# Optimization experiments

Hardware: AMD Instinct MI355X
Metric: run time of the kernel (lower is better)

The kernel has to match this reference:

```python
import jax, jax.numpy as jnp
import numpy as np

OUT, IN = 4096, 4096
B, S = 4, 2048


def setup_inputs() -> dict:
    key = jax.random.key(0)
    k1, k2, k3, k4 = jax.random.split(key, 4)
    x = jax.random.normal(k1, (B, S, IN), dtype=jnp.float32)
    # signed int8 values, stored as int32 for portability
    weight_int8 = jax.random.randint(k2, (OUT, IN), -128, 128, dtype=jnp.int32)
    # per-row dequant scale (positive, small)
    scale = jax.random.uniform(k3, (OUT,), dtype=jnp.float32) * 0.01 + 1e-4
    bias = jax.random.normal(k4, (OUT,), dtype=jnp.float32)
    return {"x": x, "weight_int8": weight_int8, "scale": scale, "bias": bias}


def reference(x, weight_int8, scale, bias):
    # dequantize: int8 -> fp, per-row scale (scale.view(-1,1) branch)
    w = weight_int8.astype(x.dtype) * scale[:, None]          # [OUT, IN]
    # F.linear(x, w, bias) = x @ w.T + bias
    out = jnp.einsum("bsi,oi->bso", x, w) + bias               # [B, S, OUT]
    return out
```

## Files before the change

kernel.cpp:

```cpp
#include <hip/hip_runtime.h>
#include <hip/hip_bf16.h>
#include <stdint.h>


#define M_TOT 8192
#define N_TOT 4096
#define K_TOT 4096

#define BM 128
#define BN 128
#define BK 32

typedef uint32_t u32;
typedef __attribute__((ext_vector_type(4))) float f32x4;
typedef __attribute__((ext_vector_type(8))) __bf16 bf16x8;

#define GLOBAL_AS __attribute__((address_space(1)))
#define LDS_AS __attribute__((address_space(3)))
#define ASYNC_COPY16(gp, lp) \
  __builtin_amdgcn_global_load_lds((GLOBAL_AS void*)(gp), (LDS_AS void*)(lp), 16, 0, 0)

__device__ __forceinline__ uint16_t bf16_rne(float f) {
  u32 u = __builtin_bit_cast(u32, f);
  u32 r = u + 0x7FFFu + ((u >> 16) & 1u);
  return (uint16_t)(r >> 16);
}

__global__ __launch_bounds__(256) void cvt_x_kernel(const float* __restrict__ x,
                                                    uint16_t* __restrict__ hi,
                                                    uint16_t* __restrict__ lo,
                                                    int n4) {
  int idx = blockIdx.x * blockDim.x + threadIdx.x;
  int stride = gridDim.x * blockDim.x;
  for (int i = idx; i < n4; i += stride) {
    float4 v = reinterpret_cast<const float4*>(x)[i];
    float fv[4] = {v.x, v.y, v.z, v.w};
    uint16_t hh[4], ll[4];
#pragma unroll
    for (int j = 0; j < 4; ++j) {
      uint16_t hb = bf16_rne(fv[j]);
      float hf = __builtin_bit_cast(float, (u32)hb << 16);
      hh[j] = hb;
      ll[j] = bf16_rne(fv[j] - hf);
    }
    uint2 hv, lv;
    hv.x = (u32)hh[0] | ((u32)hh[1] << 16);
    hv.y = (u32)hh[2] | ((u32)hh[3] << 16);
    lv.x = (u32)ll[0] | ((u32)ll[1] << 16);
    lv.y = (u32)ll[2] | ((u32)ll[3] << 16);
    reinterpret_cast<uint2*>(hi)[i] = hv;
    reinterpret_cast<uint2*>(lo)[i] = lv;
  }
}

__global__ __launch_bounds__(256) void cvt_w_kernel(const int* __restrict__ w,
                                                    uint16_t* __restrict__ wb,
                                                    int n4) {
  int idx = blockIdx.x * blockDim.x + threadIdx.x;
  int stride = gridDim.x * blockDim.x;
  for (int i = idx; i < n4; i += stride) {
    int4 v = reinterpret_cast<const int4*>(w)[i];
    uint16_t r0 = (uint16_t)(__builtin_bit_cast(u32, (float)v.x) >> 16);
    uint16_t r1 = (uint16_t)(__builtin_bit_cast(u32, (float)v.y) >> 16);
    uint16_t r2 = (uint16_t)(__builtin_bit_cast(u32, (float)v.z) >> 16);
    uint16_t r3 = (uint16_t)(__builtin_bit_cast(u32, (float)v.w) >> 16);
    uint2 rv;
    rv.x = (u32)r0 | ((u32)r1 << 16);
    rv.y = (u32)r2 | ((u32)r3 << 16);
    reinterpret_cast<uint2*>(wb)[i] = rv;
  }
}

__global__ __launch_bounds__(256, 2) void gemm_kernel(
    const uint16_t* __restrict__ xhi, const uint16_t* __restrict__ xlo,
    const uint16_t* __restrict__ wb, const float* __restrict__ scale,
    const float* __restrict__ bias, float* __restrict__ out) {
  __shared__ __align__(16) uint16_t sAhi[BM * BK];
  __shared__ __align__(16) uint16_t sAlo[BM * BK];
  __shared__ __align__(16) uint16_t sW[BN * BK];

  const int NBX = N_TOT / BN;
  const int NWG = (M_TOT / BM) * NBX;
  int wg = (int)blockIdx.x;
  wg = (wg & 7) * (NWG >> 3) + (wg >> 3);
  const int by = wg / NBX;
  const int bx = wg % NBX;
  const int m0 = by * BM;
  const int n0 = bx * BN;

  const int tid = (int)threadIdx.x;
  const int lane = tid & 63;
  const int wid = tid >> 6;
  const int wm = (wid >> 1) * 64;
  const int wn = (wid & 1) * 64;

  const int srow = lane >> 2;
  const int scol = (lane & 3) * 8;

  const int fr = lane & 15;
  const int fk = (lane >> 4) * 8;

  f32x4 acc[4][4] = {};

  for (int ks = 0; ks < K_TOT / BK; ++ks) {
    const int k0 = ks * BK;
    __syncthreads();
#pragma unroll
    for (int i = 0; i < 2; ++i) {
      const int chunk = wid * 2 + i;
      const int row = chunk * 16 + srow;
      const size_t ga = (size_t)(m0 + row) * K_TOT + (size_t)(k0 + scol);
      const size_t gw = (size_t)(n0 + row) * K_TOT + (size_t)(k0 + scol);
      ASYNC_COPY16(xhi + ga, &sAhi[chunk * 16 * BK]);
      ASYNC_COPY16(xlo + ga, &sAlo[chunk * 16 * BK]);
      ASYNC_COPY16(wb + gw, &sW[chunk * 16 * BK]);
    }
    __syncthreads();

    bf16x8 ah[4], al[4], bf[4];
#pragma unroll
    for (int m = 0; m < 4; ++m) {
      const int r = wm + m * 16 + fr;
      ah[m] = *reinterpret_cast<const bf16x8*>(&sAhi[r * BK + fk]);
      al[m] = *reinterpret_cast<const bf16x8*>(&sAlo[r * BK + fk]);
    }
#pragma unroll
    for (int n = 0; n < 4; ++n) {
      const int c = wn + n * 16 + fr;
      bf[n] = *reinterpret_cast<const bf16x8*>(&sW[c * BK + fk]);
    }
#pragma unroll
    for (int m = 0; m < 4; ++m) {
#pragma unroll
      for (int n = 0; n < 4; ++n) {
        acc[m][n] = __builtin_amdgcn_mfma_f32_16x16x32_bf16(ah[m], bf[n], acc[m][n], 0, 0, 0);
        acc[m][n] = __builtin_amdgcn_mfma_f32_16x16x32_bf16(al[m], bf[n], acc[m][n], 0, 0, 0);
      }
    }
  }

  const int fq = lane >> 4;
#pragma unroll
  for (int n = 0; n < 4; ++n) {
    const int col = n0 + wn + n * 16 + (lane & 15);
    const float sc = scale[col];
    const float bi = bias[col];
#pragma unroll
    for (int m = 0; m < 4; ++m) {
      const int rbase = m0 + wm + m * 16 + fq * 4;
#pragma unroll
      for (int j = 0; j < 4; ++j) {
        out[(size_t)(rbase + j) * N_TOT + col] = acc[m][n][j] * sc + bi;
      }
    }
  }
}

extern "C" void kernel_launch(void* const* d_in, const int* in_sizes, int n_in,
                              void* d_out, int out_size, void* d_ws, size_t ws_size,
                              hipStream_t stream) {
  const float* x = (const float*)d_in[0];
  const int* w8 = (const int*)d_in[1];
  const float* scale = (const float*)d_in[2];
  const float* bias = (const float*)d_in[3];
  float* out = (float*)d_out;

  uint16_t* xhi = (uint16_t*)d_ws;
  uint16_t* xlo = xhi + (size_t)M_TOT * K_TOT;
  uint16_t* wbf = xlo + (size_t)M_TOT * K_TOT;

  const int x_n4 = (M_TOT * K_TOT) / 4;
  const int w_n4 = (N_TOT * K_TOT) / 4;

  cvt_x_kernel<<<2048, 256, 0, stream>>>(x, xhi, xlo, x_n4);
  cvt_w_kernel<<<1024, 256, 0, stream>>>(w8, wbf, w_n4);

  const int nwg = (M_TOT / BM) * (N_TOT / BN);
  gemm_kernel<<<nwg, 256, 0, stream>>>(xhi, xlo, wbf, scale, bias, out);
}
```

Baseline: 827.3 us.

## Rewrite GEMM as 8-wave 256x256 double-buffered pipeline with swizzled LDS

The GEMM kernel moves from 128x128x32 tiles with 4 waves to 256x256x64 tiles with 8 waves in a 128KB LDS double buffer. The hi and lo halves of x become one concatenated K dimension of 8192, so each MFMA pass reads a single A operand. Global-to-LDS async loads for the next tiles are interleaved with four MFMA quadrants, using explicit waitcnt, barriers and setprio, and the LDS layout is XOR-swizzled to avoid bank conflicts. The goal is more reuse per loaded tile and overlap of memory traffic with matrix math. The cost is a fragile, hand-scheduled pipeline, the weight tiles being loaded twice, and only one workgroup fitting per CU.

```diff
diff --git a/kernel.cpp b/kernel.cpp
--- a/kernel.cpp
+++ b/kernel.cpp
@@ -6,10 +6,11 @@
 #define M_TOT 8192
 #define N_TOT 4096
 #define K_TOT 4096
-
-#define BM 128
-#define BN 128
-#define BK 32
+#define KE    8192
+#define BM 256
+#define BN 256
+#define BK 64
+#define NT (KE / BK)
 
 typedef uint32_t u32;
 typedef __attribute__((ext_vector_type(4))) float f32x4;
@@ -17,8 +18,17 @@
 
 #define GLOBAL_AS __attribute__((address_space(1)))
 #define LDS_AS __attribute__((address_space(3)))
-#define ASYNC_COPY16(gp, lp) \
-  __builtin_amdgcn_global_load_lds((GLOBAL_AS void*)(gp), (LDS_AS void*)(lp), 16, 0, 0)
+#define ASYNC16(gp, lp) \
+  __builtin_amdgcn_global_load_lds((const GLOBAL_AS void*)(gp), (LDS_AS void*)(lp), 16, 0, 0)
+
+#define FENCE asm volatile("" ::: "memory")
+#define BARRIER __builtin_amdgcn_s_barrier()
+#define LGKM0                                      \
+  do {                                             \
+    asm volatile("s_waitcnt lgkmcnt(0)" ::: "memory"); \
+    __builtin_amdgcn_sched_barrier(0);             \
+  } while (0)
+#define MFMA(a, b, c) __builtin_amdgcn_mfma_f32_16x16x32_bf16((a), (b), (c), 0, 0, 0)
 
 __device__ __forceinline__ uint16_t bf16_rne(float f) {
   u32 u = __builtin_bit_cast(u32, f);
@@ -71,89 +81,157 @@
   }
 }
 
-__global__ __launch_bounds__(256, 2) void gemm_kernel(
+__global__ __launch_bounds__(512, 2) void gemm_kernel(
     const uint16_t* __restrict__ xhi, const uint16_t* __restrict__ xlo,
-    const uint16_t* __restrict__ wb, const float* __restrict__ scale,
+    const uint16_t* __restrict__ wbf, const float* __restrict__ scale,
     const float* __restrict__ bias, float* __restrict__ out) {
-  __shared__ __align__(16) uint16_t sAhi[BM * BK];
-  __shared__ __align__(16) uint16_t sAlo[BM * BK];
-  __shared__ __align__(16) uint16_t sW[BN * BK];
+  __shared__ __align__(16) uint8_t lds[131072];
 
   const int NBX = N_TOT / BN;
   const int NWG = (M_TOT / BM) * NBX;
   int wg = (int)blockIdx.x;
   wg = (wg & 7) * (NWG >> 3) + (wg >> 3);
-  const int by = wg / NBX;
-  const int bx = wg % NBX;
-  const int m0 = by * BM;
-  const int n0 = bx * BN;
+  const int m0 = (wg / NBX) * BM;
+  const int n0 = (wg % NBX) * BN;
 
   const int tid = (int)threadIdx.x;
   const int lane = tid & 63;
   const int wid = tid >> 6;
-  const int wm = (wid >> 1) * 64;
-  const int wn = (wid & 1) * 64;
-
-  const int srow = lane >> 2;
-  const int scol = (lane & 3) * 8;
+  const int wm = (wid >> 2) * 128;
+  const int wn = (wid & 3) * 64;
+
+  const int lg = (lane << 4) ^ (lane & 32);
+  const int lrow = lg >> 6;
+  const int lcolE = (lg & 63) >> 1;
 
   const int fr = lane & 15;
   const int fk = (lane >> 4) * 8;
-
-  f32x4 acc[4][4] = {};
-
-  for (int ks = 0; ks < K_TOT / BK; ++ks) {
-    const int k0 = ks * BK;
-    __syncthreads();
-#pragma unroll
-    for (int i = 0; i < 2; ++i) {
-      const int chunk = wid * 2 + i;
-      const int row = chunk * 16 + srow;
-      const size_t ga = (size_t)(m0 + row) * K_TOT + (size_t)(k0 + scol);
-      const size_t gw = (size_t)(n0 + row) * K_TOT + (size_t)(k0 + scol);
-      ASYNC_COPY16(xhi + ga, &sAhi[chunk * 16 * BK]);
-      ASYNC_COPY16(xlo + ga, &sAlo[chunk * 16 * BK]);
-      ASYNC_COPY16(wb + gw, &sW[chunk * 16 * BK]);
+  const int inner = ((fr * 64) + (fk * 2)) ^ ((fr & 8) << 2);
+  const int abase = ((1 + (wm >> 7)) << 14) + inner;
+  const int bbase = (((wn >> 7) ? 3 : 0) << 14) + inner;
+  const int bq = (wn & 64) ? 4 : 0;
+
+#define STAGE(H, T)                                                                  \
+  do {                                                                               \
+    const int _T = (T);                                                              \
+    const uint16_t* _src;                                                            \
+    int _row0;                                                                       \
+    if ((H) == 1 || (H) == 2) {                                                      \
+      _src = (_T < 64) ? xhi : xlo;                                                  \
+      _row0 = m0 + (((H) == 2) ? 128 : 0);                                           \
+    } else {                                                                         \
+      _src = wbf;                                                                    \
+      _row0 = n0 + (((H) == 3) ? 128 : 0);                                           \
+    }                                                                                \
+    const int _k0 = (_T & 63) * BK;                                                  \
+    const uint16_t* _s = _src + (size_t)(_row0 + (wid << 4) + lrow) * K_TOT + _k0 + lcolE; \
+    uint8_t* _l = lds + (((_T) & 1) << 16) + ((H) << 14) + (wid << 11);              \
+    ASYNC16(_s, _l);                                                                 \
+    ASYNC16(_s + 32, _l + 1024);                                                     \
+  } while (0)
+
+#define RDA(m, ks) (*(const bf16x8*)(lds + bufoff + abase + ((((m) * 2) + (ks)) << 10)))
+#define RDB(n, ks) (*(const bf16x8*)(lds + bufoff + bbase + (((((n) + bq) * 2) + (ks)) << 10)))
+
+  f32x4 acc[8][4] = {};
+
+  STAGE(0, 0); STAGE(1, 0); STAGE(2, 0); STAGE(3, 0);
+  asm volatile("s_waitcnt vmcnt(4)" ::: "memory");
+  STAGE(0, 1); STAGE(1, 1); STAGE(2, 1);
+  asm volatile("s_waitcnt vmcnt(6)" ::: "memory");
+  FENCE;
+  BARRIER;
+
+  for (int t = 0; t < NT; ++t) {
+    const int bufoff = (t & 1) << 16;
+    bf16x8 b0[2][2], b1[2][2], aLo[4][2], aHi[4][2];
+
+#pragma unroll
+    for (int n = 0; n < 2; ++n) { b0[n][0] = RDB(n, 0); b0[n][1] = RDB(n, 1); }
+#pragma unroll
+    for (int n = 0; n < 2; ++n) { b1[n][0] = RDB(n + 2, 0); b1[n][1] = RDB(n + 2, 1); }
+#pragma unroll
+    for (int m = 0; m < 4; ++m) { aLo[m][0] = RDA(m, 0); aLo[m][1] = RDA(m, 1); }
+    if (t + 1 < NT) STAGE(3, t + 1);
+    FENCE; BARRIER; LGKM0;
+    __builtin_amdgcn_s_setprio(1);
+#pragma unroll
+    for (int m = 0; m < 4; ++m)
+#pragma unroll
+      for (int n = 0; n < 2; ++n) {
+        acc[m][n] = MFMA(aLo[m][0], b0[n][0], acc[m][n]);
+        acc[m][n] = MFMA(aLo[m][1], b0[n][1], acc[m][n]);
+      }
+    __builtin_amdgcn_s_setprio(0);
+    FENCE; BARRIER;
+
+#pragma unroll
+    for (int m = 0; m < 4; ++m) { aHi[m][0] = RDA(m + 4, 0); aHi[m][1] = RDA(m + 4, 1); }
+    if (t + 2 < NT) STAGE(0, t + 2);
+    FENCE; BARRIER; LGKM0;
+    __builtin_amdgcn_s_setprio(1);
+#pragma unroll
+    for (int m = 0; m < 4; ++m)
+#pragma unroll
+      for (int n = 0; n < 2; ++n) {
+        acc[m][n + 2] = MFMA(aLo[m][0], b1[n][0], acc[m][n + 2]);
+        acc[m][n + 2] = MFMA(aLo[m][1], b1[n][1], acc[m][n + 2]);
+      }
+    __builtin_amdgcn_s_setprio(0);
+    FENCE; BARRIER;
+
+    if (t + 2 < NT) STAGE(1, t + 2);
+    FENCE; BARRIER; LGKM0;
+    __builtin_amdgcn_s_setprio(1);
+#pragma unroll
+    for (int m = 0; m < 4; ++m)
+#pragma unroll
+      for (int n = 0; n < 2; ++n) {
+        acc[m + 4][n] = MFMA(aHi[m][0], b0[n][0], acc[m + 4][n]);
+        acc[m + 4][n] = MFMA(aHi[m][1], b0[n][1], acc[m + 4][n]);
+      }
+    __builtin_amdgcn_s_setprio(0);
+    FENCE; BARRIER;
+
+    if (t + 2 < NT) STAGE(2, t + 2);
+    FENCE; BARRIER; LGKM0;
+    __builtin_amdgcn_s_setprio(1);
+#pragma unroll
+    for (int m = 0; m < 4; ++m)
+#pragma unroll
+      for (int n = 0; n < 2; ++n) {
+        acc[m + 4][n + 2] = MFMA(aHi[m][0], b1[n][0], acc[m + 4][n + 2]);
+        acc[m + 4][n + 2] = MFMA(aHi[m][1], b1[n][1], acc[m + 4][n + 2]);
+      }
+    __builtin_amdgcn_s_setprio(0);
+    if (t < NT - 1) {
+      if (t == NT - 2) {
+        asm volatile("s_waitcnt vmcnt(0)" ::: "memory");
+      } else {
+        asm volatile("s_waitcnt vmcnt(6)" ::: "memory");
+      }
+      FENCE; BARRIER;
     }
-    __syncthreads();
-
-    bf16x8 ah[4], al[4], bf[4];
-#pragma unroll
-    for (int m = 0; m < 4; ++m) {
-      const int r = wm + m * 16 + fr;
-      ah[m] = *reinterpret_cast<const bf16x8*>(&sAhi[r * BK + fk]);
-      al[m] = *reinterpret_cast<const bf16x8*>(&sAlo[r * BK + fk]);
+  }
+
+  const int fq = lane >> 4;
+#pragma unroll
+  for (int n = 0; n < 4; ++n) {
+    const int col = n0 + wn + n * 16 + fr;
+    const float sc = scale[col];
+    const float bb = bias[col];
+#pragma unroll
+    for (int m = 0; m < 8; ++m) {
+      const int rb = m0 + wm + m * 16 + fq * 4;
+#pragma unroll
+      for (int j = 0; j < 4; ++j) {
+        out[(size_t)(rb + j) * N_TOT + col] = acc[m][n][j] * sc + bb;
+      }
     }
-#pragma unroll
-    for (int n = 0; n < 4; ++n) {
-      const int c = wn + n * 16 + fr;
-      bf[n] = *reinterpret_cast<const bf16x8*>(&sW[c * BK + fk]);
-    }
-#pragma unroll
-    for (int m = 0; m < 4; ++m) {
-#pragma unroll
-      for (int n = 0; n < 4; ++n) {
-        acc[m][n] = __builtin_amdgcn_mfma_f32_16x16x32_bf16(ah[m], bf[n], acc[m][n], 0, 0, 0);
-        acc[m][n] = __builtin_amdgcn_mfma_f32_16x16x32_bf16(al[m], bf[n], acc[m][n], 0, 0, 0);
-      }
-    }
-  }
-
-  const int fq = lane >> 4;
-#pragma unroll
-  for (int n = 0; n < 4; ++n) {
-    const int col = n0 + wn + n * 16 + (lane & 15);
-    const float sc = scale[col];
-    const float bi = bias[col];
-#pragma unroll
-    for (int m = 0; m < 4; ++m) {
-      const int rbase = m0 + wm + m * 16 + fq * 4;
-#pragma unroll
-      for (int j = 0; j < 4; ++j) {
-        out[(size_t)(rbase + j) * N_TOT + col] = acc[m][n][j] * sc + bi;
-      }
-    }
-  }
+  }
+#undef STAGE
+#undef RDA
+#undef RDB
 }
 
 extern "C" void kernel_launch(void* const* d_in, const int* in_sizes, int n_in,
@@ -176,5 +254,5 @@
   cvt_w_kernel<<<1024, 256, 0, stream>>>(w8, wbf, w_n4);
 
   const int nwg = (M_TOT / BM) * (N_TOT / BN);
-  gemm_kernel<<<nwg, 256, 0, stream>>>(xhi, xlo, wbf, scale, bias, out);
-}
+  gemm_kernel<<<nwg, 512, 0, stream>>>(xhi, xlo, wbf, scale, bias, out);
+}
```

New measurement: 714.8 us. 13.6% less time.
